# Performance work log

Measured on AMD Instinct MI355X. Metric: run time of the kernel, lower is better.

## Reference

```python
import jax, jax.numpy as jnp
import numpy as np

N_NODES = 8192
IN_FEATS, H_FEATS, NUM_CLASSES = 512, 256, 16


def _glorot(key, shape):
    fan_in, fan_out = shape[0], shape[1]
    limit = float(np.sqrt(6.0 / (fan_in + fan_out)))
    return jax.random.uniform(key, shape, jnp.float32, -limit, limit)


def setup_inputs() -> dict:
    key = jax.random.key(0)
    ks = jax.random.split(key, 16)
    return {
        "x": jax.random.normal(ks[0], (N_NODES, IN_FEATS), jnp.float32),
        "w1": _glorot(ks[1], (IN_FEATS, H_FEATS)), "b1": jnp.zeros((H_FEATS,), jnp.float32),
        "w2": _glorot(ks[2], (H_FEATS, H_FEATS)), "b2": jnp.zeros((H_FEATS,), jnp.float32),
        "w3": _glorot(ks[3], (H_FEATS, 32)),      "b3": jnp.zeros((32,), jnp.float32),
        "t": _glorot(ks[4], (1, 1)), "theta": _glorot(ks[5], (1, 1)),
        "gw1": _glorot(ks[6], (32, 16)), "gb1": jnp.zeros((16,), jnp.float32),
        "gw2": _glorot(ks[7], (16, 8)),  "gb2": jnp.zeros((8,), jnp.float32),
        "lw1": _glorot(ks[8], (8, 16)),  "lb1": jnp.zeros((16,), jnp.float32),
        "lw2": _glorot(ks[9], (16, NUM_CLASSES)), "lb2": jnp.zeros((NUM_CLASSES,), jnp.float32),
    }


def _pairwise_dist(h):
    # Euclidean cdist(h, h): [N, N], stable sqrt with zero subgradient at d=0
    sq = jnp.sum(h * h, axis=1)
    d2 = jnp.maximum(sq[:, None] + sq[None, :] - 2.0 * (h @ h.T), 0.0)
    return jnp.where(d2 > 0.0, jnp.sqrt(jnp.where(d2 > 0.0, d2, 1.0)), 0.0)


def reference(x, w1, b1, w2, b2, w3, b3, t, theta, gw1, gb1, gw2, gb2, lw1, lb1, lw2, lb2):
    n = x.shape[0]
    # MLP encoder (dropout is eval-mode identity)
    h = jax.nn.relu(x @ w1 + b1)
    h = jax.nn.relu(h @ w2 + b2)
    h = h @ w3 + b3                                  # [N, 32]
    # latent dense graph: A = sigmoid(t * (cdist + theta)); all entries > 0 -> fully dense graph
    A = jax.nn.sigmoid(t[0, 0] * (_pairwise_dist(h) + theta[0, 0]))   # [N, N]
    inv_deg = 1.0 / n                                # norm='right', in-degree == N for dense graph
    # GraphConv: dst aggregates sum_src A[src,dst] * (h[src] @ W) then right-normalizes
    h = jax.nn.relu((A.T @ (h @ gw1)) * inv_deg + gb1)   # [N, 16]
    h = jax.nn.relu((A.T @ (h @ gw2)) * inv_deg + gb2)   # [N, 8]
    h = jax.nn.relu(h @ lw1 + lb1)
    return h @ lw2 + lb2                             # [N, num_classes]
```

## Files before the change

kernel.cpp:

```cpp
#include <hip/hip_runtime.h>

typedef __attribute__((ext_vector_type(8))) short short8;
typedef __attribute__((ext_vector_type(4))) float f32x4;
typedef __attribute__((ext_vector_type(2))) unsigned int u32x2;
typedef unsigned short u16;
typedef unsigned int u32;

#define MFMA16 __builtin_amdgcn_mfma_f32_16x16x32_bf16

constexpr int NCH = 16;
constexpr int NJT = 8192 / 64 / NCH;

__device__ __forceinline__ void lds_order_fence() { asm volatile("" ::: "memory"); }

__device__ __forceinline__ u16 f2bf(float f) {
    u32 u = __builtin_bit_cast(u32, f);
    return (u16)((u + 0x7FFFu + ((u >> 16) & 1u)) >> 16);
}

__device__ __forceinline__ void split2(float f, u16& hi, u16& lo) {
    u32 u = __builtin_bit_cast(u32, f);
    hi = (u16)(u >> 16);
    float hf = __builtin_bit_cast(float, u & 0xFFFF0000u);
    float r = f - hf;
    lo = (u16)(__builtin_bit_cast(u32, r) >> 16);
}

__device__ __forceinline__ int swzA(int row, int slot) {
    return row * 64 + ((slot ^ ((row >> 1) & 3)) << 4);
}

__global__ void __launch_bounds__(256) k_tr(const float* __restrict__ w, float* __restrict__ wt,
                                            int K, int N) {
    int idx = blockIdx.x * 256 + threadIdx.x;
    if (idx >= K * N) return;
    int k = idx / N, n = idx - k * N;
    wt[n * K + k] = w[idx];
}

template <int K, int BN, bool RELU>
__global__ void __launch_bounds__(256, 2) k_gemm(const float* __restrict__ A,
                                                 const float* __restrict__ Bt,
                                                 const float* __restrict__ bias,
                                                 float* __restrict__ C, const int N) {
    constexpr int NT = BN / 16;
    __shared__ __align__(16) char smem[16384];
    char* const Ah = smem;
    char* const Al = smem + 4096;
    char* const Bh = smem + 8192;
    char* const Bl = smem + 12288;
    const int tid = threadIdx.x, lane = tid & 63, w = tid >> 6;
    const int frow = lane & 15, fg = lane >> 4;
    const int m0 = blockIdx.x * 64, n0 = blockIdx.y * BN;
    const int srow = tid >> 2, sc = tid & 3;
    const int swa = swzA(srow, sc);
    const bool doB = (BN == 64) || (tid < 128);
    const float* gA = A + (m0 + srow) * K + sc * 8;
    const float* gB = Bt + (n0 + srow) * K + sc * 8;

    f32x4 acc[NT];
    float bv[NT];
#pragma unroll
    for (int nt = 0; nt < NT; nt++) {
        acc[nt] = {0.f, 0.f, 0.f, 0.f};
        bv[nt] = bias[n0 + nt * 16 + frow];
    }
    const int fra = swzA(w * 16 + frow, fg);
    int frb[NT];
#pragma unroll
    for (int nt = 0; nt < NT; nt++) frb[nt] = swzA(nt * 16 + frow, fg);

    for (int k0 = 0; k0 < K; k0 += 32) {
        f32x4 a0 = *(const f32x4*)(gA + k0);
        f32x4 a1 = *(const f32x4*)(gA + k0 + 4);
        f32x4 b0 = {0.f, 0.f, 0.f, 0.f}, b1 = {0.f, 0.f, 0.f, 0.f};
        if (doB) {
            b0 = *(const f32x4*)(gB + k0);
            b1 = *(const f32x4*)(gB + k0 + 4);
        }
        __syncthreads();
        {
            short8 ah8, al8;
#pragma unroll
            for (int i = 0; i < 4; i++) { u16 hh, ll; split2(a0[i], hh, ll); ah8[i] = (short)hh; al8[i] = (short)ll; }
#pragma unroll
            for (int i = 0; i < 4; i++) { u16 hh, ll; split2(a1[i], hh, ll); ah8[4 + i] = (short)hh; al8[4 + i] = (short)ll; }
            *(short8*)(Ah + swa) = ah8;
            *(short8*)(Al + swa) = al8;
        }
        if (doB) {
            short8 bh8, bl8;
#pragma unroll
            for (int i = 0; i < 4; i++) { u16 hh, ll; split2(b0[i], hh, ll); bh8[i] = (short)hh; bl8[i] = (short)ll; }
#pragma unroll
            for (int i = 0; i < 4; i++) { u16 hh, ll; split2(b1[i], hh, ll); bh8[4 + i] = (short)hh; bl8[4 + i] = (short)ll; }
            *(short8*)(Bh + swa) = bh8;
            *(short8*)(Bl + swa) = bl8;
        }
        __syncthreads();
        const short8 afh = *(const short8*)(Ah + fra);
        const short8 afl = *(const short8*)(Al + fra);
#pragma unroll
        for (int nt = 0; nt < NT; nt++) {
            const short8 bfh = *(const short8*)(Bh + frb[nt]);
            const short8 bfl = *(const short8*)(Bl + frb[nt]);
            acc[nt] = MFMA16(afh, bfh, acc[nt], 0, 0, 0);
            acc[nt] = MFMA16(afh, bfl, acc[nt], 0, 0, 0);
            acc[nt] = MFMA16(afl, bfh, acc[nt], 0, 0, 0);
        }
    }
#pragma unroll
    for (int nt = 0; nt < NT; nt++) {
#pragma unroll
        for (int r = 0; r < 4; r++) {
            float v = acc[nt][r] + bv[nt];
            if (RELU) v = fmaxf(v, 0.f);
            C[(m0 + w * 16 + fg * 4 + r) * N + (n0 + nt * 16 + frow)] = v;
        }
    }
}

__global__ void __launch_bounds__(256) k_post(const float* __restrict__ H,
                                              const float* __restrict__ gw1,
                                              u16* __restrict__ hhi, u16* __restrict__ hlo,
                                              float* __restrict__ sqv, u16* __restrict__ B1t) {
    __shared__ float gs[512];
    const int tid = threadIdx.x;
    gs[tid] = gw1[tid];
    gs[tid + 256] = gw1[tid + 256];
    __syncthreads();
    const int j = blockIdx.x * 256 + tid;
    float h[32];
#pragma unroll
    for (int q = 0; q < 8; q++) {
        f32x4 v = *(const f32x4*)(H + j * 32 + q * 4);
        h[q * 4 + 0] = v[0]; h[q * 4 + 1] = v[1]; h[q * 4 + 2] = v[2]; h[q * 4 + 3] = v[3];
    }
    float s = 0.f;
#pragma unroll
    for (int k = 0; k < 32; k++) s = fmaf(h[k], h[k], s);
    sqv[j] = s;
#pragma unroll
    for (int q = 0; q < 4; q++) {
        short8 vh, vl;
#pragma unroll
        for (int e = 0; e < 8; e++) {
            u16 hh, ll;
            split2(h[q * 8 + e], hh, ll);
            vh[e] = (short)hh; vl[e] = (short)ll;
        }
        *(short8*)(hhi + j * 32 + q * 8) = vh;
        *(short8*)(hlo + j * 32 + q * 8) = vl;
    }
    const float inv = 0.0001220703125f;
#pragma unroll
    for (int f = 0; f < 16; f++) {
        float a = 0.f;
#pragma unroll
        for (int k = 0; k < 32; k++) a = fmaf(h[k], gs[k * 16 + f], a);
        B1t[f * 8192 + j] = f2bf(a * inv);
    }
}

template <bool DIAG>
__device__ __forceinline__ void ew_pack(char* astr, int awoff, const f32x4 s, const f32x4 sq4,
                                        float sq_i, float c0, float c1, int jloc, int il) {
    float p[4];
#pragma unroll
    for (int r = 0; r < 4; r++) {
        float d2 = fmaf(s[r], -2.f, sq_i + sq4[r]);
        d2 = fmaxf(d2, 0.f);
        float d = __builtin_amdgcn_sqrtf(d2);
        if (DIAG) {
            if (jloc + r == il) d = 0.f;
        }
        const float z = fmaf(d, c1, c0);
        p[r] = __builtin_amdgcn_rcpf(1.f + __builtin_amdgcn_exp2f(z));
    }
    u32 w0, w1;
    asm("v_cvt_pk_bf16_f32 %0, %1, %2" : "=v"(w0) : "v"(p[0]), "v"(p[1]));
    asm("v_cvt_pk_bf16_f32 %0, %1, %2" : "=v"(w1) : "v"(p[2]), "v"(p[3]));
    u32x2 pk = {w0, w1};
    *(u32x2*)(astr + awoff) = pk;
}

__global__ void __launch_bounds__(256) k_agg(const u16* __restrict__ hhi, const u16* __restrict__ hlo,
                                             const float* __restrict__ sqv, const u16* __restrict__ Bt,
                                             float* __restrict__ P,
                                             const float* __restrict__ tp, const float* __restrict__ thp) {
    __shared__ __align__(16) char smem[24576];
    char* const bufh = smem;
    char* const bufl = smem + 8192;
    char* const astr0 = smem + 16384;

    const int tid = threadIdx.x, lane = tid & 63, w = tid >> 6;
    const int frow = lane & 15, fg = lane >> 4;
    const int dstbase = blockIdx.x * 64;
    const int chunk = blockIdx.y;
    const float t = tp[0], th = thp[0];
    const float c1 = -t * 1.44269504088896340736f;
    const float c0 = c1 * th;
    char* const astr = astr0 + w * 2048;

    const int srow = tid >> 2, sc = tid & 3;
    const int swa = swzA(srow, sc);

    const int igf = dstbase + w * 16 + frow;
    const short8 hdh = *(const short8*)(hhi + igf * 32 + fg * 8);
    const short8 hdl = *(const short8*)(hlo + igf * 32 + fg * 8);
    const float sq_i = sqv[igf];
    const int il = w * 16 + frow;

    int awo[4], ard[2];
#pragma unroll
    for (int jj = 0; jj < 4; jj++)
        awo[jj] = frow * 128 + (((2 * jj + (fg >> 1)) ^ (frow & 7)) << 4) + ((fg & 1) << 3);
#pragma unroll
    for (int h = 0; h < 2; h++) ard[h] = frow * 128 + (((4 * h + fg) ^ (frow & 7)) << 4);

    f32x4 outacc = {0.f, 0.f, 0.f, 0.f};

    const int jt0 = chunk * NJT;
    short8 pvh = *(const short8*)(hhi + ((jt0 * 64) + srow) * 32 + sc * 8);
    short8 pvl = *(const short8*)(hlo + ((jt0 * 64) + srow) * 32 + sc * 8);
    *(short8*)(bufh + swa) = pvh;
    *(short8*)(bufl + swa) = pvl;
    if (NJT > 1) {
        const int jn = (jt0 + 1) * 64;
        pvh = *(const short8*)(hhi + (jn + srow) * 32 + sc * 8);
        pvl = *(const short8*)(hlo + (jn + srow) * 32 + sc * 8);
    }

    for (int it = 0; it < NJT; ++it) {
        const int b = it & 1;
        const int jbase = (jt0 + it) * 64;
        __syncthreads();
        if (it + 1 < NJT) {
            *(short8*)(bufh + (b ^ 1) * 4096 + swa) = pvh;
            *(short8*)(bufl + (b ^ 1) * 4096 + swa) = pvl;
        }
        if (it + 2 < NJT) {
            const int jn = (jt0 + it + 2) * 64;
            pvh = *(const short8*)(hhi + (jn + srow) * 32 + sc * 8);
            pvl = *(const short8*)(hlo + (jn + srow) * 32 + sc * 8);
        }
        char* const bh = bufh + b * 4096;
        char* const bl = bufl + b * 4096;
        const bool diag = (jbase == dstbase);
#pragma unroll
        for (int h = 0; h < 2; ++h) {
            const short8 hs0h = *(const short8*)(bh + swzA(h * 32 + frow, fg));
            const short8 hs0l = *(const short8*)(bl + swzA(h * 32 + frow, fg));
            const short8 hs1h = *(const short8*)(bh + swzA(h * 32 + 16 + frow, fg));
            const short8 hs1l = *(const short8*)(bl + swzA(h * 32 + 16 + frow, fg));
            const f32x4 sq0 = *(const f32x4*)(sqv + jbase + h * 32 + fg * 4);
            const f32x4 sq1 = *(const f32x4*)(sqv + jbase + h * 32 + 16 + fg * 4);
            const short8 bfh = *(const short8*)(Bt + frow * 8192 + jbase + h * 32 + fg * 8);
            f32x4 s0 = {0.f, 0.f, 0.f, 0.f}, s1 = {0.f, 0.f, 0.f, 0.f};
            s0 = MFMA16(hs0h, hdh, s0, 0, 0, 0);
            s0 = MFMA16(hs0h, hdl, s0, 0, 0, 0);
            s0 = MFMA16(hs0l, hdh, s0, 0, 0, 0);
            s1 = MFMA16(hs1h, hdh, s1, 0, 0, 0);
            s1 = MFMA16(hs1h, hdl, s1, 0, 0, 0);
            s1 = MFMA16(hs1l, hdh, s1, 0, 0, 0);
            lds_order_fence();
            if (diag) {
                ew_pack<true>(astr, awo[2 * h], s0, sq0, sq_i, c0, c1, (2 * h) * 16 + fg * 4, il);
                ew_pack<true>(astr, awo[2 * h + 1], s1, sq1, sq_i, c0, c1, (2 * h + 1) * 16 + fg * 4, il);
            } else {
                ew_pack<false>(astr, awo[2 * h], s0, sq0, sq_i, c0, c1, 0, -1);
                ew_pack<false>(astr, awo[2 * h + 1], s1, sq1, sq_i, c0, c1, 0, -1);
            }
            lds_order_fence();
            const short8 af = *(const short8*)(astr + ard[h]);
            outacc = MFMA16(af, bfh, outacc, 0, 0, 0);
        }
    }
#pragma unroll
    for (int r = 0; r < 4; r++) {
        const int ig = dstbase + w * 16 + fg * 4 + r;
        P[(chunk * 8192 + ig) * 16 + frow] = outacc[r];
    }
}

__global__ void __launch_bounds__(256) k_reduce1(const float* __restrict__ P,
                                                 const float* __restrict__ gw2,
                                                 const float* __restrict__ gb1,
                                                 u16* __restrict__ B2t) {
    __shared__ float gs[128];
    const int tid = threadIdx.x;
    if (tid < 128) gs[tid] = gw2[tid];
    __syncthreads();
    const int j = blockIdx.x * 256 + tid;
    float g[16];
#pragma unroll
    for (int q = 0; q < 4; q++) {
        f32x4 v = *(const f32x4*)(P + j * 16 + q * 4);
        g[q * 4 + 0] = v[0]; g[q * 4 + 1] = v[1]; g[q * 4 + 2] = v[2]; g[q * 4 + 3] = v[3];
    }
#pragma unroll
    for (int c = 1; c < NCH; c++) {
#pragma unroll
        for (int q = 0; q < 4; q++) {
            f32x4 v = *(const f32x4*)(P + (c * 8192 + j) * 16 + q * 4);
            g[q * 4 + 0] += v[0]; g[q * 4 + 1] += v[1]; g[q * 4 + 2] += v[2]; g[q * 4 + 3] += v[3];
        }
    }
#pragma unroll
    for (int f = 0; f < 16; f++) g[f] = fmaxf(g[f] + gb1[f], 0.f);
    const float inv = 0.0001220703125f;
#pragma unroll
    for (int f2 = 0; f2 < 8; f2++) {
        float a = 0.f;
#pragma unroll
        for (int k = 0; k < 16; k++) a = fmaf(g[k], gs[k * 8 + f2], a);
        B2t[f2 * 8192 + j] = f2bf(a * inv);
    }
#pragma unroll
    for (int f2 = 8; f2 < 16; f2++) B2t[f2 * 8192 + j] = 0;
}

__global__ void __launch_bounds__(256) k_final(const float* __restrict__ P,
                                               const float* __restrict__ gb2,
                                               const float* __restrict__ lw1,
                                               const float* __restrict__ lb1,
                                               const float* __restrict__ lw2,
                                               const float* __restrict__ lb2,
                                               float* __restrict__ out) {
    __shared__ float s1[128], s2[256];
    const int tid = threadIdx.x;
    if (tid < 128) s1[tid] = lw1[tid];
    s2[tid] = lw2[tid];
    __syncthreads();
    const int j = blockIdx.x * 256 + tid;
    float g[8];
#pragma unroll
    for (int q = 0; q < 2; q++) {
        f32x4 v = *(const f32x4*)(P + j * 16 + q * 4);
        g[q * 4 + 0] = v[0]; g[q * 4 + 1] = v[1]; g[q * 4 + 2] = v[2]; g[q * 4 + 3] = v[3];
    }
#pragma unroll
    for (int c = 1; c < NCH; c++) {
#pragma unroll
        for (int q = 0; q < 2; q++) {
            f32x4 v = *(const f32x4*)(P + (c * 8192 + j) * 16 + q * 4);
            g[q * 4 + 0] += v[0]; g[q * 4 + 1] += v[1]; g[q * 4 + 2] += v[2]; g[q * 4 + 3] += v[3];
        }
    }
#pragma unroll
    for (int f = 0; f < 8; f++) g[f] = fmaxf(g[f] + gb2[f], 0.f);
    float l1[16];
#pragma unroll
    for (int f = 0; f < 16; f++) {
        float a = lb1[f];
#pragma unroll
        for (int k = 0; k < 8; k++) a = fmaf(g[k], s1[k * 16 + f], a);
        l1[f] = fmaxf(a, 0.f);
    }
#pragma unroll
    for (int q = 0; q < 4; q++) {
        f32x4 v;
#pragma unroll
        for (int e = 0; e < 4; e++) {
            const int f = q * 4 + e;
            float a = lb2[f];
#pragma unroll
            for (int k = 0; k < 16; k++) a = fmaf(l1[k], s2[k * 16 + f], a);
            v[e] = a;
        }
        *(f32x4*)(out + j * 16 + q * 4) = v;
    }
}

extern "C" void kernel_launch(void* const* d_in, const int* in_sizes, int n_in,
                              void* d_out, int out_size, void* d_ws, size_t ws_size,
                              hipStream_t stream) {
    (void)in_sizes; (void)n_in; (void)out_size; (void)ws_size;
    const float* x   = (const float*)d_in[0];
    const float* w1  = (const float*)d_in[1];
    const float* b1  = (const float*)d_in[2];
    const float* w2  = (const float*)d_in[3];
    const float* b2  = (const float*)d_in[4];
    const float* w3  = (const float*)d_in[5];
    const float* b3  = (const float*)d_in[6];
    const float* t   = (const float*)d_in[7];
    const float* th  = (const float*)d_in[8];
    const float* gw1 = (const float*)d_in[9];
    const float* gb1 = (const float*)d_in[10];
    const float* gw2 = (const float*)d_in[11];
    const float* gb2 = (const float*)d_in[12];
    const float* lw1 = (const float*)d_in[13];
    const float* lb1 = (const float*)d_in[14];
    const float* lw2 = (const float*)d_in[15];
    const float* lb2 = (const float*)d_in[16];

    char* ws = (char*)d_ws;
    float* wt1 = (float*)(ws + 0);
    float* wt2 = (float*)(ws + 524288);
    float* wt3 = (float*)(ws + 786432);
    float* H1  = (float*)(ws + 819200);
    float* P   = (float*)(ws + 819200);
    float* H2  = (float*)(ws + 9207808);
    float* H   = (float*)(ws + 17596416);
    u16*   hhi = (u16*)(ws + 18644992);
    u16*   hlo = (u16*)(ws + 19169280);
    float* sqv = (float*)(ws + 19693568);
    u16*   B1t = (u16*)(ws + 19726336);
    u16*   B2t = (u16*)(ws + 19988480);

    k_tr<<<(512 * 256 + 255) / 256, 256, 0, stream>>>(w1, wt1, 512, 256);
    k_tr<<<(256 * 256 + 255) / 256, 256, 0, stream>>>(w2, wt2, 256, 256);
    k_tr<<<(256 * 32 + 255) / 256, 256, 0, stream>>>(w3, wt3, 256, 32);

    k_gemm<512, 64, true ><<<dim3(128, 4), 256, 0, stream>>>(x,  wt1, b1, H1, 256);
    k_gemm<256, 64, true ><<<dim3(128, 4), 256, 0, stream>>>(H1, wt2, b2, H2, 256);
    k_gemm<256, 32, false><<<dim3(128, 1), 256, 0, stream>>>(H2, wt3, b3, H, 32);

    k_post<<<32, 256, 0, stream>>>(H, gw1, hhi, hlo, sqv, B1t);

    k_agg<<<dim3(128, NCH), 256, 0, stream>>>(hhi, hlo, sqv, B1t, P, t, th);
    k_reduce1<<<32, 256, 0, stream>>>(P, gw2, gb1, B2t);
    k_agg<<<dim3(128, NCH), 256, 0, stream>>>(hhi, hlo, sqv, B2t, P, t, th);
    k_final<<<32, 256, 0, stream>>>(P, gb2, lw1, lb1, lw2, lb2, (float*)d_out);
}
```

Baseline: 133.1 us.

## Widen aggregation blocks to 128 destination rows and hoist per-tile global loads

The aggregation kernel now runs 512 threads, with each block covering 128 destination rows instead of 64. The staged source tile in LDS is shared across twice as many waves, and only the first 256 threads do the staging. The per-tile sq and B fragment global loads are hoisted ahead of the barrier so their latency overlaps the sync. This halves source-tile global traffic per destination row, but the grid has half as many blocks and each block needs more LDS, which may reduce occupancy and load balance.

```diff
diff --git a/kernel.cpp b/kernel.cpp
--- a/kernel.cpp
+++ b/kernel.cpp
@@ -184,32 +184,34 @@
     *(u32x2*)(astr + awoff) = pk;
 }
 
-__global__ void __launch_bounds__(256) k_agg(const u16* __restrict__ hhi, const u16* __restrict__ hlo,
+__global__ void __launch_bounds__(512) k_agg(const u16* __restrict__ hhi, const u16* __restrict__ hlo,
                                              const float* __restrict__ sqv, const u16* __restrict__ Bt,
                                              float* __restrict__ P,
                                              const float* __restrict__ tp, const float* __restrict__ thp) {
-    __shared__ __align__(16) char smem[24576];
+    __shared__ __align__(16) char smem[32768];
     char* const bufh = smem;
     char* const bufl = smem + 8192;
     char* const astr0 = smem + 16384;
 
     const int tid = threadIdx.x, lane = tid & 63, w = tid >> 6;
     const int frow = lane & 15, fg = lane >> 4;
-    const int dstbase = blockIdx.x * 64;
+    const int dstbase = blockIdx.x * 128;
     const int chunk = blockIdx.y;
     const float t = tp[0], th = thp[0];
     const float c1 = -t * 1.44269504088896340736f;
     const float c0 = c1 * th;
     char* const astr = astr0 + w * 2048;
 
-    const int srow = tid >> 2, sc = tid & 3;
+    const bool stager = (tid < 256);
+    const int srow = (tid & 255) >> 2, sc = tid & 3;
     const int swa = swzA(srow, sc);
 
     const int igf = dstbase + w * 16 + frow;
     const short8 hdh = *(const short8*)(hhi + igf * 32 + fg * 8);
     const short8 hdl = *(const short8*)(hlo + igf * 32 + fg * 8);
     const float sq_i = sqv[igf];
-    const int il = w * 16 + frow;
+    const int jdiag = dstbase + ((w >> 2) << 6);
+    const int il = (w & 3) * 16 + frow;
 
     int awo[4], ard[2];
 #pragma unroll
@@ -219,43 +221,52 @@
     for (int h = 0; h < 2; h++) ard[h] = frow * 128 + (((4 * h + fg) ^ (frow & 7)) << 4);
 
     f32x4 outacc = {0.f, 0.f, 0.f, 0.f};
+    const u16* bgp = Bt + frow * 8192;
 
     const int jt0 = chunk * NJT;
-    short8 pvh = *(const short8*)(hhi + ((jt0 * 64) + srow) * 32 + sc * 8);
-    short8 pvl = *(const short8*)(hlo + ((jt0 * 64) + srow) * 32 + sc * 8);
-    *(short8*)(bufh + swa) = pvh;
-    *(short8*)(bufl + swa) = pvl;
-    if (NJT > 1) {
-        const int jn = (jt0 + 1) * 64;
-        pvh = *(const short8*)(hhi + (jn + srow) * 32 + sc * 8);
-        pvl = *(const short8*)(hlo + (jn + srow) * 32 + sc * 8);
+    short8 pvh, pvl;
+    if (stager) {
+        pvh = *(const short8*)(hhi + ((jt0 * 64) + srow) * 32 + sc * 8);
+        pvl = *(const short8*)(hlo + ((jt0 * 64) + srow) * 32 + sc * 8);
+        *(short8*)(bufh + swa) = pvh;
+        *(short8*)(bufl + swa) = pvl;
+        if (NJT > 1) {
+            const int jn = (jt0 + 1) * 64;
+            pvh = *(const short8*)(hhi + (jn + srow) * 32 + sc * 8);
+            pvl = *(const short8*)(hlo + (jn + srow) * 32 + sc * 8);
+        }
     }
 
     for (int it = 0; it < NJT; ++it) {
         const int b = it & 1;
         const int jbase = (jt0 + it) * 64;
+        f32x4 sqg[4];
+        short8 bfg[2];
+#pragma unroll
+        for (int q = 0; q < 4; q++) sqg[q] = *(const f32x4*)(sqv + jbase + q * 16 + fg * 4);
+#pragma unroll
+        for (int q = 0; q < 2; q++) bfg[q] = *(const short8*)(bgp + jbase + q * 32 + fg * 8);
         __syncthreads();
-        if (it + 1 < NJT) {
-            *(short8*)(bufh + (b ^ 1) * 4096 + swa) = pvh;
-            *(short8*)(bufl + (b ^ 1) * 4096 + swa) = pvl;
-        }
-        if (it + 2 < NJT) {
-            const int jn = (jt0 + it + 2) * 64;
-            pvh = *(const short8*)(hhi + (jn + srow) * 32 + sc * 8);
-            pvl = *(const short8*)(hlo + (jn + srow) * 32 + sc * 8);
+        if (stager) {
+            if (it + 1 < NJT) {
+                *(short8*)(bufh + (b ^ 1) * 4096 + swa) = pvh;
+                *(short8*)(bufl + (b ^ 1) * 4096 + swa) = pvl;
+            }
+            if (it + 2 < NJT) {
+                const int jn = (jt0 + it + 2) * 64;
+                pvh = *(const short8*)(hhi + (jn + srow) * 32 + sc * 8);
+                pvl = *(const short8*)(hlo + (jn + srow) * 32 + sc * 8);
+            }
         }
         char* const bh = bufh + b * 4096;
         char* const bl = bufl + b * 4096;
-        const bool diag = (jbase == dstbase);
+        const bool diag = (jbase == jdiag);
 #pragma unroll
         for (int h = 0; h < 2; ++h) {
             const short8 hs0h = *(const short8*)(bh + swzA(h * 32 + frow, fg));
             const short8 hs0l = *(const short8*)(bl + swzA(h * 32 + frow, fg));
             const short8 hs1h = *(const short8*)(bh + swzA(h * 32 + 16 + frow, fg));
             const short8 hs1l = *(const short8*)(bl + swzA(h * 32 + 16 + frow, fg));
-            const f32x4 sq0 = *(const f32x4*)(sqv + jbase + h * 32 + fg * 4);
-            const f32x4 sq1 = *(const f32x4*)(sqv + jbase + h * 32 + 16 + fg * 4);
-            const short8 bfh = *(const short8*)(Bt + frow * 8192 + jbase + h * 32 + fg * 8);
             f32x4 s0 = {0.f, 0.f, 0.f, 0.f}, s1 = {0.f, 0.f, 0.f, 0.f};
             s0 = MFMA16(hs0h, hdh, s0, 0, 0, 0);
             s0 = MFMA16(hs0h, hdl, s0, 0, 0, 0);
@@ -265,15 +276,15 @@
             s1 = MFMA16(hs1l, hdh, s1, 0, 0, 0);
             lds_order_fence();
             if (diag) {
-                ew_pack<true>(astr, awo[2 * h], s0, sq0, sq_i, c0, c1, (2 * h) * 16 + fg * 4, il);
-                ew_pack<true>(astr, awo[2 * h + 1], s1, sq1, sq_i, c0, c1, (2 * h + 1) * 16 + fg * 4, il);
+                ew_pack<true>(astr, awo[2 * h], s0, sqg[2 * h], sq_i, c0, c1, (2 * h) * 16 + fg * 4, il);
+                ew_pack<true>(astr, awo[2 * h + 1], s1, sqg[2 * h + 1], sq_i, c0, c1, (2 * h + 1) * 16 + fg * 4, il);
             } else {
-                ew_pack<false>(astr, awo[2 * h], s0, sq0, sq_i, c0, c1, 0, -1);
-                ew_pack<false>(astr, awo[2 * h + 1], s1, sq1, sq_i, c0, c1, 0, -1);
+                ew_pack<false>(astr, awo[2 * h], s0, sqg[2 * h], sq_i, c0, c1, 0, -1);
+                ew_pack<false>(astr, awo[2 * h + 1], s1, sqg[2 * h + 1], sq_i, c0, c1, 0, -1);
             }
             lds_order_fence();
             const short8 af = *(const short8*)(astr + ard[h]);
-            outacc = MFMA16(af, bfh, outacc, 0, 0, 0);
+            outacc = MFMA16(af, bfg[h], outacc, 0, 0, 0);
         }
     }
 #pragma unroll
@@ -418,8 +429,8 @@
 
     k_post<<<32, 256, 0, stream>>>(H, gw1, hhi, hlo, sqv, B1t);
 
-    k_agg<<<dim3(128, NCH), 256, 0, stream>>>(hhi, hlo, sqv, B1t, P, t, th);
+    k_agg<<<dim3(64, NCH), 512, 0, stream>>>(hhi, hlo, sqv, B1t, P, t, th);
     k_reduce1<<<32, 256, 0, stream>>>(P, gw2, gb1, B2t);
-    k_agg<<<dim3(128, NCH), 256, 0, stream>>>(hhi, hlo, sqv, B2t, P, t, th);
+    k_agg<<<dim3(64, NCH), 512, 0, stream>>>(hhi, hlo, sqv, B2t, P, t, th);
     k_final<<<32, 256, 0, stream>>>(P, gb2, lw1, lb1, lw2, lb2, (float*)d_out);
 }
```

Measured after the change: 134.4 us. About the same (+1.0%).
